# Performance work log

Hardware: AMD Instinct MI355X
Metric: run time of the kernel (lower is better)

Reference implementation:

```python
import jax, jax.numpy as jnp
import numpy as np

NUM_HEAD = 16
MODEL_DIM = 1024
K_DIM = MODEL_DIM // NUM_HEAD
LN_EPS = 1e-5


def setup_inputs() -> dict:
    key = jax.random.key(0)
    ks = jax.random.split(key, 9)
    B, N, D = 4, 2048, MODEL_DIM
    scale = 1.0 / np.sqrt(D)
    return {
        "q": jax.random.normal(ks[0], (B, N, D), dtype=jnp.float32),
        "k": jax.random.normal(ks[1], (B, N, D), dtype=jnp.float32),
        "v": jax.random.normal(ks[2], (B, N, D), dtype=jnp.float32),
        "Wq": jax.random.normal(ks[3], (D, D), dtype=jnp.float32) * scale,
        "Wk": jax.random.normal(ks[4], (D, D), dtype=jnp.float32) * scale,
        "Wv": jax.random.normal(ks[5], (D, D), dtype=jnp.float32) * scale,
        "Wo": jax.random.normal(ks[6], (D, D), dtype=jnp.float32) * scale,
        "gamma": jnp.ones((D,), dtype=jnp.float32),
        "beta": jnp.zeros((D,), dtype=jnp.float32),
    }


def reference(q, k, v, Wq, Wk, Wv, Wo, gamma, beta):
    B, N, D = q.shape
    H, Dh = NUM_HEAD, K_DIM
    # QKV projections (torch Linear: x @ W.T), then split heads -> [B,H,N,Dh]
    qs = (q @ Wq.T).reshape(B, N, H, Dh).transpose(0, 2, 1, 3)
    ks = (k @ Wk.T).reshape(B, N, H, Dh).transpose(0, 2, 1, 3)
    vs = (v @ Wv.T).reshape(B, N, H, Dh).transpose(0, 2, 1, 3)
    # scaled dot-product attention
    scores = jnp.einsum("bhqd,bhkd->bhqk", qs, ks) / jnp.sqrt(jnp.float32(Dh))
    probs = jax.nn.softmax(scores, axis=-1)
    attn = jnp.einsum("bhqk,bhkd->bhqd", probs, vs)
    # merge heads and output projection
    attn = attn.transpose(0, 2, 1, 3).reshape(B, N, D)
    out = attn @ Wo.T + q  # residual
    # LayerNorm
    mu = jnp.mean(out, axis=-1, keepdims=True)
    var = jnp.var(out, axis=-1, keepdims=True)
    out = (out - mu) * jax.lax.rsqrt(var + LN_EPS) * gamma + beta
    return out
```

## Files before the change

kernel.cpp:

```cpp
#include <hip/hip_runtime.h>
#include <cstdint>
#include <math.h>

typedef __bf16 bf16x8 __attribute__((ext_vector_type(8)));
typedef float f32x2 __attribute__((ext_vector_type(2)));
typedef float f32x4 __attribute__((ext_vector_type(4)));
typedef float f32x16 __attribute__((ext_vector_type(16)));
typedef int i32x2 __attribute__((ext_vector_type(2)));
typedef unsigned u32x4 __attribute__((ext_vector_type(4)));
typedef unsigned short u16;

#define B_ 4
#define N_ 2048
#define D_ 1024
#define H_ 16
#define DH_ 64
#define M_ (B_*N_)

#define QSCALE (0.125f * 1.44269504088896f)

typedef const void __attribute__((address_space(1))) gvoid;
typedef void __attribute__((address_space(3))) lvoid;

__device__ __forceinline__ void gload16(const void* g, void* l) {
  __builtin_amdgcn_global_load_lds((gvoid*)g, (lvoid*)l, 16, 0, 0);
}

__device__ __forceinline__ u16 cvt_bf(float f) {
  __bf16 h = (__bf16)f;
  return *(u16*)&h;
}

__device__ __forceinline__ unsigned cvt_pk(float lo, float hi) {
  unsigned r;
  asm("v_cvt_pk_bf16_f32 %0, %1, %2" : "=v"(r) : "v"(lo), "v"(hi));
  return r;
}

__device__ __forceinline__ i32x2 pl32swap(unsigned a, unsigned b) {
  return __builtin_amdgcn_permlane32_swap((int)a, (int)b, false, false);
}

__device__ __forceinline__ f32x2 pk_add(f32x2 a, f32x2 b) {
  f32x2 d;
  asm("v_pk_add_f32 %0, %1, %2" : "=v"(d) : "v"(a), "v"(b));
  return d;
}
__device__ __forceinline__ f32x2 pk_mul(f32x2 a, f32x2 b) {
  f32x2 d;
  asm("v_pk_mul_f32 %0, %1, %2" : "=v"(d) : "v"(a), "v"(b));
  return d;
}

__global__ __launch_bounds__(256) void cast_all(
    const float* __restrict__ q, const float* __restrict__ k, const float* __restrict__ v,
    const float* __restrict__ wq, const float* __restrict__ wk,
    const float* __restrict__ wv, const float* __restrict__ wo,
    u16* __restrict__ oq, u16* __restrict__ ok, u16* __restrict__ ov,
    u16* __restrict__ owq, u16* __restrict__ owk, u16* __restrict__ owv, u16* __restrict__ owo) {
  const int nb = (B_*N_*D_)/4;
  const int nw = (D_*D_)/4;
  int i = blockIdx.x * 256 + threadIdx.x;
  const float* s; u16* d;
  if (i < 3*nb) {
    if (i < nb)        { s = q; d = oq; }
    else if (i < 2*nb) { s = k; d = ok; i -= nb; }
    else               { s = v; d = ov; i -= 2*nb; }
  } else {
    i -= 3*nb;
    if (i < nw)        { s = wq; d = owq; }
    else if (i < 2*nw) { s = wk; d = owk; i -= nw; }
    else if (i < 3*nw) { s = wv; d = owv; i -= 2*nw; }
    else               { s = wo; d = owo; i -= 3*nw; }
  }
  float4 x = ((const float4*)s)[i];
  ushort4 y;
  y.x = cvt_bf(x.x); y.y = cvt_bf(x.y); y.z = cvt_bf(x.z); y.w = cvt_bf(x.w);
  ((ushort4*)d)[i] = y;
}

__global__ __launch_bounds__(256) void gemm_qkv(
    const u16* __restrict__ Aq, const u16* __restrict__ Ak, const u16* __restrict__ Av,
    const u16* __restrict__ Wq, const u16* __restrict__ Wk, const u16* __restrict__ Wv,
    u16* __restrict__ Oq, u16* __restrict__ Ok, u16* __restrict__ Ov)
{
  __shared__ __align__(16) u16 As[128*64];
  __shared__ __align__(16) u16 Bs[128*64];
  const int z = blockIdx.z;
  const u16* A = (z == 0) ? Aq : (z == 1) ? Ak : Av;
  const u16* W = (z == 0) ? Wq : (z == 1) ? Wk : Wv;
  u16* obf     = (z == 0) ? Oq : (z == 1) ? Ok : Ov;
  const float oscale = (z == 0) ? QSCALE : 1.0f;

  const int t = threadIdx.x;
  const int lane = t & 63;
  const int w = t >> 6;
  const int wr = w >> 1, wc = w & 1;
  const int m0 = blockIdx.x * 128;
  const int n0 = blockIdx.y * 128;
  f32x4 acc[4][4] = {};

  const int srow = t >> 3;
  const int scb = (t & 7) ^ (srow & 7);
  const int fr = lane & 15;
  const int fg = lane >> 4;
  const int fs7 = fr & 7;

  for (int k0 = 0; k0 < 1024; k0 += 64) {
#pragma unroll
    for (int p = 0; p < 4; ++p) {
      int r = p*32 + srow;
      gload16(A + (size_t)(m0 + r)*1024 + k0 + scb*8, &As[(p*256 + t)*8]);
      gload16(W + (size_t)(n0 + r)*1024 + k0 + scb*8, &Bs[(p*256 + t)*8]);
    }
    __syncthreads();
#pragma unroll
    for (int ks = 0; ks < 2; ++ks) {
      bf16x8 af[4], bfr[4];
#pragma unroll
      for (int i = 0; i < 4; ++i) {
        int ra = wr*64 + i*16 + fr;
        af[i]  = *(const bf16x8*)&As[ra*64 + (((ks*4 + fg) ^ fs7) * 8)];
        int rb = wc*64 + i*16 + fr;
        bfr[i] = *(const bf16x8*)&Bs[rb*64 + (((ks*4 + fg) ^ fs7) * 8)];
      }
#pragma unroll
      for (int i = 0; i < 4; ++i)
#pragma unroll
        for (int j = 0; j < 4; ++j)
          acc[i][j] = __builtin_amdgcn_mfma_f32_16x16x32_bf16(af[i], bfr[j], acc[i][j], 0, 0, 0);
    }
    __syncthreads();
  }

#pragma unroll
  for (int i = 0; i < 4; ++i) {
#pragma unroll
    for (int j = 0; j < 4; ++j) {
#pragma unroll
      for (int jj = 0; jj < 4; ++jj) {
        int row = m0 + wr*64 + i*16 + fg*4 + jj;
        int col = n0 + wc*64 + j*16 + fr;
        float val = acc[i][j][jj];
        int b = row >> 11, n = row & 2047, h = col >> 6, dh = col & 63;
        if (z != 2) {
          obf[(((size_t)(b*H_ + h))*N_ + n)*DH_ + dh] = cvt_bf(val * oscale);
        } else {
          obf[(((size_t)(b*H_ + h))*DH_ + dh)*N_ + n] = cvt_bf(val);
        }
      }
    }
  }
}

__global__ __launch_bounds__(256) void gemm_out(
    const u16* __restrict__ A, const u16* __restrict__ W,
    const float* __restrict__ resid, float* __restrict__ ofp)
{
  __shared__ __align__(16) u16 As[128*64];
  __shared__ __align__(16) u16 Bs[128*64];
  const int t = threadIdx.x;
  const int lane = t & 63;
  const int w = t >> 6;
  const int wr = w >> 1, wc = w & 1;
  const int m0 = blockIdx.x * 128;
  const int n0 = blockIdx.y * 128;
  f32x4 acc[4][4] = {};

  const int srow = t >> 3;
  const int scb = (t & 7) ^ (srow & 7);
  const int fr = lane & 15;
  const int fg = lane >> 4;
  const int fs7 = fr & 7;

  for (int k0 = 0; k0 < 1024; k0 += 64) {
#pragma unroll
    for (int p = 0; p < 4; ++p) {
      int r = p*32 + srow;
      gload16(A + (size_t)(m0 + r)*1024 + k0 + scb*8, &As[(p*256 + t)*8]);
      gload16(W + (size_t)(n0 + r)*1024 + k0 + scb*8, &Bs[(p*256 + t)*8]);
    }
    __syncthreads();
#pragma unroll
    for (int ks = 0; ks < 2; ++ks) {
      bf16x8 af[4], bfr[4];
#pragma unroll
      for (int i = 0; i < 4; ++i) {
        int ra = wr*64 + i*16 + fr;
        af[i]  = *(const bf16x8*)&As[ra*64 + (((ks*4 + fg) ^ fs7) * 8)];
        int rb = wc*64 + i*16 + fr;
        bfr[i] = *(const bf16x8*)&Bs[rb*64 + (((ks*4 + fg) ^ fs7) * 8)];
      }
#pragma unroll
      for (int i = 0; i < 4; ++i)
#pragma unroll
        for (int j = 0; j < 4; ++j)
          acc[i][j] = __builtin_amdgcn_mfma_f32_16x16x32_bf16(af[i], bfr[j], acc[i][j], 0, 0, 0);
    }
    __syncthreads();
  }

#pragma unroll
  for (int i = 0; i < 4; ++i)
#pragma unroll
    for (int j = 0; j < 4; ++j)
#pragma unroll
      for (int jj = 0; jj < 4; ++jj) {
        int row = m0 + wr*64 + i*16 + fg*4 + jj;
        int col = n0 + wc*64 + j*16 + fr;
        size_t idx = (size_t)row*1024 + col;
        ofp[idx] = acc[i][j][jj] + resid[idx];
      }
}

__device__ __forceinline__ f32x2 sp2(const f32x16& S, int i) {
  f32x2 r; r.x = S[2*i]; r.y = S[2*i + 1]; return r;
}
__device__ __forceinline__ void exp2v(f32x16& S) {
#pragma unroll
  for (int r = 0; r < 16; ++r) S[r] = __builtin_amdgcn_exp2f(S[r]);
}
__device__ __forceinline__ f32x2 sumtree(const f32x16& S0, const f32x16& S1) {
  f32x2 a0 = pk_add(sp2(S0,0), sp2(S0,1));
  f32x2 a1 = pk_add(sp2(S0,2), sp2(S0,3));
  f32x2 a2 = pk_add(sp2(S0,4), sp2(S0,5));
  f32x2 a3 = pk_add(sp2(S0,6), sp2(S0,7));
  f32x2 b0 = pk_add(sp2(S1,0), sp2(S1,1));
  f32x2 b1 = pk_add(sp2(S1,2), sp2(S1,3));
  f32x2 b2 = pk_add(sp2(S1,4), sp2(S1,5));
  f32x2 b3 = pk_add(sp2(S1,6), sp2(S1,7));
  a0 = pk_add(a0, a1); a2 = pk_add(a2, a3);
  b0 = pk_add(b0, b1); b2 = pk_add(b2, b3);
  a0 = pk_add(a0, a2); b0 = pk_add(b0, b2);
  return pk_add(a0, b0);
}
__device__ __forceinline__ void buildP(const f32x16& S, bf16x8* pf) {
  unsigned w0 = cvt_pk(S[0], S[1]),  w1 = cvt_pk(S[2], S[3]);
  unsigned w2 = cvt_pk(S[4], S[5]),  w3 = cvt_pk(S[6], S[7]);
  i32x2 A2 = pl32swap(w0, w2), B2 = pl32swap(w1, w3);
  u32x4 f0 = { (unsigned)A2.x, (unsigned)B2.x, (unsigned)A2.y, (unsigned)B2.y };
  pf[0] = __builtin_bit_cast(bf16x8, f0);
  unsigned w4 = cvt_pk(S[8], S[9]),   w5 = cvt_pk(S[10], S[11]);
  unsigned w6 = cvt_pk(S[12], S[13]), w7 = cvt_pk(S[14], S[15]);
  i32x2 C2 = pl32swap(w4, w6), D2 = pl32swap(w5, w7);
  u32x4 f1 = { (unsigned)C2.x, (unsigned)D2.x, (unsigned)C2.y, (unsigned)D2.y };
  pf[1] = __builtin_bit_cast(bf16x8, f1);
}

__global__ __launch_bounds__(256, 2) void flash_attn(
    const u16* __restrict__ Qs, const u16* __restrict__ Ks,
    const u16* __restrict__ VTs, u16* __restrict__ ctx)
{
  __shared__ __align__(16) u16 Klds[2][64*64];
  __shared__ __align__(16) u16 Vlds[2][64*64];
  const int t = threadIdx.x;
  const int lane = t & 63;
  const int w = t >> 6;
  const int l31 = lane & 31;
  const int h = lane >> 5;
  const int bh = blockIdx.x;
  const int q0 = blockIdx.y * 256 + w * 64;
  const u16* Qbh = Qs  + (size_t)bh * N_ * DH_;
  const u16* Kbh = Ks  + (size_t)bh * N_ * DH_;
  const u16* Vbh = VTs + (size_t)bh * DH_ * N_;

  bf16x8 qfA[4], qfB[4];
#pragma unroll
  for (int dd = 0; dd < 4; ++dd) {
    qfA[dd] = *(const bf16x8*)&Qbh[(size_t)(q0 + l31)*64 + dd*16 + h*8];
    qfB[dd] = *(const bf16x8*)&Qbh[(size_t)(q0 + 32 + l31)*64 + dd*16 + h*8];
  }

  f32x2 lA = {0.f, 0.f}, lB = {0.f, 0.f};
  f32x16 OA0 = {}, OA1 = {}, OB0 = {}, OB1 = {};

  const int srow = t >> 3;
  const int scb  = (t & 7) ^ (srow & 7);
  const u16* ksrc = Kbh + (size_t)srow*64 + scb*8;
  const u16* vsrc = Vbh + (size_t)srow*N_ + scb*8;

  auto stage = [&](int buf, int kv) {
#pragma unroll
    for (int p = 0; p < 2; ++p) {
      gload16(ksrc + (size_t)(kv + p*32)*64, &Klds[buf][(p*256 + t)*8]);
      gload16(vsrc + kv + (size_t)(p*32)*N_, &Vlds[buf][(p*256 + t)*8]);
    }
  };

  const int l7 = l31 & 7;

  stage(0, 0);
  __syncthreads();
  int cur = 0;

  for (int kv0 = 0; kv0 < N_; kv0 += 64) {
    if (kv0 + 64 < N_) stage(cur ^ 1, kv0 + 64);

    bf16x8 kf0[4], kf1[4];
#pragma unroll
    for (int dd = 0; dd < 4; ++dd) {
      int cb = ((dd*2 + h) ^ l7) * 8;
      kf0[dd] = *(const bf16x8*)&Klds[cur][l31*64 + cb];
      kf1[dd] = *(const bf16x8*)&Klds[cur][(32 + l31)*64 + cb];
    }
    f32x16 SA0 = {}, SA1 = {}, SB0 = {}, SB1 = {};
    __builtin_amdgcn_s_setprio(1);
#pragma unroll
    for (int dd = 0; dd < 4; ++dd) {
      SA0 = __builtin_amdgcn_mfma_f32_32x32x16_bf16(kf0[dd], qfA[dd], SA0, 0, 0, 0);
      SA1 = __builtin_amdgcn_mfma_f32_32x32x16_bf16(kf1[dd], qfA[dd], SA1, 0, 0, 0);
    }
#pragma unroll
    for (int dd = 0; dd < 4; ++dd) {
      SB0 = __builtin_amdgcn_mfma_f32_32x32x16_bf16(kf0[dd], qfB[dd], SB0, 0, 0, 0);
      SB1 = __builtin_amdgcn_mfma_f32_32x32x16_bf16(kf1[dd], qfB[dd], SB1, 0, 0, 0);
    }
    __builtin_amdgcn_s_setprio(0);

    exp2v(SA0); exp2v(SA1);
    bf16x8 pfA[4];
    buildP(SA0, &pfA[0]);
    buildP(SA1, &pfA[2]);

    bf16x8 vf0[4], vf1[4];
#pragma unroll
    for (int ks = 0; ks < 4; ++ks) {
      int cb = ((ks*2 + h) ^ l7) * 8;
      vf0[ks] = *(const bf16x8*)&Vlds[cur][l31*64 + cb];
      vf1[ks] = *(const bf16x8*)&Vlds[cur][(32 + l31)*64 + cb];
    }
    __builtin_amdgcn_s_setprio(1);
#pragma unroll
    for (int ks = 0; ks < 4; ++ks) {
      OA0 = __builtin_amdgcn_mfma_f32_32x32x16_bf16(vf0[ks], pfA[ks], OA0, 0, 0, 0);
      OA1 = __builtin_amdgcn_mfma_f32_32x32x16_bf16(vf1[ks], pfA[ks], OA1, 0, 0, 0);
    }
    __builtin_amdgcn_s_setprio(0);
    lA = pk_add(lA, sumtree(SA0, SA1));

    exp2v(SB0); exp2v(SB1);
    bf16x8 pfB[4];
    buildP(SB0, &pfB[0]);
    buildP(SB1, &pfB[2]);
    __builtin_amdgcn_s_setprio(1);
#pragma unroll
    for (int ks = 0; ks < 4; ++ks) {
      OB0 = __builtin_amdgcn_mfma_f32_32x32x16_bf16(vf0[ks], pfB[ks], OB0, 0, 0, 0);
      OB1 = __builtin_amdgcn_mfma_f32_32x32x16_bf16(vf1[ks], pfB[ks], OB1, 0, 0, 0);
    }
    __builtin_amdgcn_s_setprio(0);
    lB = pk_add(lB, sumtree(SB0, SB1));

    __syncthreads();
    cur ^= 1;
  }

  int b = bh >> 4, hh = bh & 15;
  {
    float lps = lA.x + lA.y;
    i32x2 lsw = pl32swap(__float_as_uint(lps), __float_as_uint(lps));
    float ltot = __uint_as_float((unsigned)lsw.x) + __uint_as_float((unsigned)lsw.y);
    float linv = __builtin_amdgcn_rcpf(ltot);
    f32x2 li2; li2.x = linv; li2.y = linv;
    unsigned* crow = (unsigned*)(ctx + ((size_t)b*N_ + (q0 + l31))*D_ + hh*64);
#pragma unroll
    for (int rp = 0; rp < 8; ++rp) {
      int r = rp*2;
      int d0 = (r & 3) + 8*(r >> 2) + 4*h;
      f32x2 o0 = pk_mul(sp2(OA0, rp), li2);
      f32x2 o1 = pk_mul(sp2(OA1, rp), li2);
      crow[d0 >> 1]        = cvt_pk(o0.x, o0.y);
      crow[(d0 + 32) >> 1] = cvt_pk(o1.x, o1.y);
    }
  }
  {
    float lps = lB.x + lB.y;
    i32x2 lsw = pl32swap(__float_as_uint(lps), __float_as_uint(lps));
    float ltot = __uint_as_float((unsigned)lsw.x) + __uint_as_float((unsigned)lsw.y);
    float linv = __builtin_amdgcn_rcpf(ltot);
    f32x2 li2; li2.x = linv; li2.y = linv;
    unsigned* crow = (unsigned*)(ctx + ((size_t)b*N_ + (q0 + 32 + l31))*D_ + hh*64);
#pragma unroll
    for (int rp = 0; rp < 8; ++rp) {
      int r = rp*2;
      int d0 = (r & 3) + 8*(r >> 2) + 4*h;
      f32x2 o0 = pk_mul(sp2(OB0, rp), li2);
      f32x2 o1 = pk_mul(sp2(OB1, rp), li2);
      crow[d0 >> 1]        = cvt_pk(o0.x, o0.y);
      crow[(d0 + 32) >> 1] = cvt_pk(o1.x, o1.y);
    }
  }
}

__global__ __launch_bounds__(256) void ln_fwd(float* __restrict__ io,
    const float* __restrict__ gamma, const float* __restrict__ beta)
{
  __shared__ float red[4];
  const int t = threadIdx.x;
  const int lane = t & 63, w = t >> 6;
  float4* row = (float4*)(io + (size_t)blockIdx.x * 1024);
  float4 x = row[t];
  float s = x.x + x.y + x.z + x.w;
#pragma unroll
  for (int m = 1; m < 64; m <<= 1) s += __shfl_xor(s, m);
  if (lane == 0) red[w] = s;
  __syncthreads();
  float mean = (red[0] + red[1] + red[2] + red[3]) * (1.f/1024.f);
  __syncthreads();
  float dx0 = x.x - mean, dx1 = x.y - mean, dx2 = x.z - mean, dx3 = x.w - mean;
  float sq = dx0*dx0 + dx1*dx1 + dx2*dx2 + dx3*dx3;
#pragma unroll
  for (int m = 1; m < 64; m <<= 1) sq += __shfl_xor(sq, m);
  if (lane == 0) red[w] = sq;
  __syncthreads();
  float var = (red[0] + red[1] + red[2] + red[3]) * (1.f/1024.f);
  float rstd = rsqrtf(var + 1e-5f);
  float4 g = ((const float4*)gamma)[t];
  float4 bb = ((const float4*)beta)[t];
  float4 y;
  y.x = dx0*rstd*g.x + bb.x;
  y.y = dx1*rstd*g.y + bb.y;
  y.z = dx2*rstd*g.z + bb.z;
  y.w = dx3*rstd*g.w + bb.w;
  row[t] = y;
}

extern "C" void kernel_launch(void* const* d_in, const int* in_sizes, int n_in,
                              void* d_out, int out_size, void* d_ws, size_t ws_size,
                              hipStream_t stream) {
  const float* q     = (const float*)d_in[0];
  const float* k     = (const float*)d_in[1];
  const float* v     = (const float*)d_in[2];
  const float* Wq    = (const float*)d_in[3];
  const float* Wk    = (const float*)d_in[4];
  const float* Wv    = (const float*)d_in[5];
  const float* Wo    = (const float*)d_in[6];
  const float* gamma = (const float*)d_in[7];
  const float* beta  = (const float*)d_in[8];
  float* out = (float*)d_out;

  char* ws = (char*)d_ws;
  const size_t MB = 1024*1024;
  u16* qb  = (u16*)(ws + 0*MB);
  u16* kb  = (u16*)(ws + 16*MB);
  u16* vb  = (u16*)(ws + 32*MB);
  u16* Wqb = (u16*)(ws + 48*MB);
  u16* Wkb = (u16*)(ws + 50*MB);
  u16* Wvb = (u16*)(ws + 52*MB);
  u16* Wob = (u16*)(ws + 54*MB);
  u16* Qs  = (u16*)(ws + 56*MB);
  u16* Ks  = (u16*)(ws + 72*MB);
  u16* VTs = (u16*)(ws + 88*MB);
  u16* ctx = (u16*)(ws + 0*MB);

  const int ntot4 = 3*((B_*N_*D_)/4) + 4*((D_*D_)/4);
  cast_all<<<ntot4/256, 256, 0, stream>>>(q, k, v, Wq, Wk, Wv, Wo,
                                          qb, kb, vb, Wqb, Wkb, Wvb, Wob);

  dim3 gproj(M_/128, D_/128, 3);
  gemm_qkv<<<gproj, 256, 0, stream>>>(qb, kb, vb, Wqb, Wkb, Wvb, Qs, Ks, VTs);

  flash_attn<<<dim3(B_*H_, N_/256), 256, 0, stream>>>(Qs, Ks, VTs, ctx);

  gemm_out<<<dim3(M_/128, D_/128), 256, 0, stream>>>(ctx, Wob, q, out);

  ln_fwd<<<M_, 256, 0, stream>>>(out, gamma, beta);
}
```

Before: 223.6 us.

## Fuse fp32 activation cast into QKV GEMM and double flash-attn KV tile

Removes the separate bf16 cast of q/k/v activations: the QKV GEMM now loads fp32 A tiles into LDS and converts to bf16 when building MFMA fragments, so only the weights are cast up front. This skips writing and re-reading about 48MB of bf16 copies, at the cost of twice the A-tile LDS traffic and extra convert instructions inside the GEMM inner loop. Separately, flash attention now stages 128 keys per iteration instead of 64, halving barrier count at the cost of double the LDS footprint, which may reduce occupancy.

```diff
diff --git a/kernel.cpp b/kernel.cpp
--- a/kernel.cpp
+++ b/kernel.cpp
@@ -52,27 +52,17 @@
   return d;
 }
 
-__global__ __launch_bounds__(256) void cast_all(
-    const float* __restrict__ q, const float* __restrict__ k, const float* __restrict__ v,
-    const float* __restrict__ wq, const float* __restrict__ wk,
-    const float* __restrict__ wv, const float* __restrict__ wo,
-    u16* __restrict__ oq, u16* __restrict__ ok, u16* __restrict__ ov,
-    u16* __restrict__ owq, u16* __restrict__ owk, u16* __restrict__ owv, u16* __restrict__ owo) {
-  const int nb = (B_*N_*D_)/4;
+__global__ __launch_bounds__(256) void cast_w(
+    const float* __restrict__ a, const float* __restrict__ b,
+    const float* __restrict__ c, const float* __restrict__ e,
+    u16* __restrict__ oa, u16* __restrict__ ob, u16* __restrict__ oc, u16* __restrict__ oe) {
   const int nw = (D_*D_)/4;
   int i = blockIdx.x * 256 + threadIdx.x;
   const float* s; u16* d;
-  if (i < 3*nb) {
-    if (i < nb)        { s = q; d = oq; }
-    else if (i < 2*nb) { s = k; d = ok; i -= nb; }
-    else               { s = v; d = ov; i -= 2*nb; }
-  } else {
-    i -= 3*nb;
-    if (i < nw)        { s = wq; d = owq; }
-    else if (i < 2*nw) { s = wk; d = owk; i -= nw; }
-    else if (i < 3*nw) { s = wv; d = owv; i -= 2*nw; }
-    else               { s = wo; d = owo; i -= 3*nw; }
-  }
+  if (i < nw)        { s = a; d = oa; }
+  else if (i < 2*nw) { s = b; d = ob; i -= nw; }
+  else if (i < 3*nw) { s = c; d = oc; i -= 2*nw; }
+  else               { s = e; d = oe; i -= 3*nw; }
   float4 x = ((const float4*)s)[i];
   ushort4 y;
   y.x = cvt_bf(x.x); y.y = cvt_bf(x.y); y.z = cvt_bf(x.z); y.w = cvt_bf(x.w);
@@ -80,16 +70,16 @@
 }
 
 __global__ __launch_bounds__(256) void gemm_qkv(
-    const u16* __restrict__ Aq, const u16* __restrict__ Ak, const u16* __restrict__ Av,
+    const float* __restrict__ Aq, const float* __restrict__ Ak, const float* __restrict__ Av,
     const u16* __restrict__ Wq, const u16* __restrict__ Wk, const u16* __restrict__ Wv,
     u16* __restrict__ Oq, u16* __restrict__ Ok, u16* __restrict__ Ov)
 {
-  __shared__ __align__(16) u16 As[128*64];
+  __shared__ __align__(16) float As32[128*64];
   __shared__ __align__(16) u16 Bs[128*64];
   const int z = blockIdx.z;
-  const u16* A = (z == 0) ? Aq : (z == 1) ? Ak : Av;
-  const u16* W = (z == 0) ? Wq : (z == 1) ? Wk : Wv;
-  u16* obf     = (z == 0) ? Oq : (z == 1) ? Ok : Ov;
+  const float* A = (z == 0) ? Aq : (z == 1) ? Ak : Av;
+  const u16* W  = (z == 0) ? Wq : (z == 1) ? Wk : Wv;
+  u16* obf      = (z == 0) ? Oq : (z == 1) ? Ok : Ov;
   const float oscale = (z == 0) ? QSCALE : 1.0f;
 
   const int t = threadIdx.x;
@@ -102,17 +92,20 @@
 
   const int srow = t >> 3;
   const int scb = (t & 7) ^ (srow & 7);
+  const int arow = t >> 4;
+  const int asb  = (t & 15) ^ arow;
+
   const int fr = lane & 15;
   const int fg = lane >> 4;
   const int fs7 = fr & 7;
 
   for (int k0 = 0; k0 < 1024; k0 += 64) {
 #pragma unroll
-    for (int p = 0; p < 4; ++p) {
-      int r = p*32 + srow;
-      gload16(A + (size_t)(m0 + r)*1024 + k0 + scb*8, &As[(p*256 + t)*8]);
-      gload16(W + (size_t)(n0 + r)*1024 + k0 + scb*8, &Bs[(p*256 + t)*8]);
-    }
+    for (int p = 0; p < 4; ++p)
+      gload16(W + (size_t)(n0 + p*32 + srow)*1024 + k0 + scb*8, &Bs[(p*256 + t)*8]);
+#pragma unroll
+    for (int p = 0; p < 8; ++p)
+      gload16(A + (size_t)(m0 + p*16 + arow)*1024 + k0 + asb*4, &As32[(p*256 + t)*4]);
     __syncthreads();
 #pragma unroll
     for (int ks = 0; ks < 2; ++ks) {
@@ -120,7 +113,13 @@
 #pragma unroll
       for (int i = 0; i < 4; ++i) {
         int ra = wr*64 + i*16 + fr;
-        af[i]  = *(const bf16x8*)&As[ra*64 + (((ks*4 + fg) ^ fs7) * 8)];
+        int b0 = (ks*4 + fg) * 2;
+        int r15 = ra & 15;
+        f32x4 lo = *(const f32x4*)&As32[ra*64 + ((b0 ^ r15) * 4)];
+        f32x4 hi = *(const f32x4*)&As32[ra*64 + (((b0 + 1) ^ r15) * 4)];
+        u32x4 pk = { cvt_pk(lo.x, lo.y), cvt_pk(lo.z, lo.w),
+                     cvt_pk(hi.x, hi.y), cvt_pk(hi.z, hi.w) };
+        af[i] = __builtin_bit_cast(bf16x8, pk);
         int rb = wc*64 + i*16 + fr;
         bfr[i] = *(const bf16x8*)&Bs[rb*64 + (((ks*4 + fg) ^ fs7) * 8)];
       }
@@ -251,8 +250,8 @@
     const u16* __restrict__ Qs, const u16* __restrict__ Ks,
     const u16* __restrict__ VTs, u16* __restrict__ ctx)
 {
-  __shared__ __align__(16) u16 Klds[2][64*64];
-  __shared__ __align__(16) u16 Vlds[2][64*64];
+  __shared__ __align__(16) u16 Klds[2][128*64];
+  __shared__ __align__(16) u16 Vlds[2][64*128];
   const int t = threadIdx.x;
   const int lane = t & 63;
   const int w = t >> 6;
@@ -274,82 +273,90 @@
   f32x2 lA = {0.f, 0.f}, lB = {0.f, 0.f};
   f32x16 OA0 = {}, OA1 = {}, OB0 = {}, OB1 = {};
 
-  const int srow = t >> 3;
-  const int scb  = (t & 7) ^ (srow & 7);
-  const u16* ksrc = Kbh + (size_t)srow*64 + scb*8;
-  const u16* vsrc = Vbh + (size_t)srow*N_ + scb*8;
+  const int krow = t >> 3;
+  const int kcb  = (t & 7) ^ (krow & 7);
+  const int vrow = t >> 4;
+  const int vcb  = (t & 15) ^ vrow;
+  const u16* ksrc = Kbh + (size_t)krow*64 + kcb*8;
+  const u16* vsrc = Vbh + (size_t)vrow*N_ + vcb*8;
 
   auto stage = [&](int buf, int kv) {
 #pragma unroll
-    for (int p = 0; p < 2; ++p) {
+    for (int p = 0; p < 4; ++p)
       gload16(ksrc + (size_t)(kv + p*32)*64, &Klds[buf][(p*256 + t)*8]);
-      gload16(vsrc + kv + (size_t)(p*32)*N_, &Vlds[buf][(p*256 + t)*8]);
-    }
+#pragma unroll
+    for (int p = 0; p < 4; ++p)
+      gload16(vsrc + kv + (size_t)(p*16)*N_, &Vlds[buf][(p*256 + t)*8]);
   };
 
   const int l7 = l31 & 7;
+  const int l15 = l31 & 15;
 
   stage(0, 0);
   __syncthreads();
   int cur = 0;
 
-  for (int kv0 = 0; kv0 < N_; kv0 += 64) {
-    if (kv0 + 64 < N_) stage(cur ^ 1, kv0 + 64);
-
-    bf16x8 kf0[4], kf1[4];
-#pragma unroll
-    for (int dd = 0; dd < 4; ++dd) {
-      int cb = ((dd*2 + h) ^ l7) * 8;
-      kf0[dd] = *(const bf16x8*)&Klds[cur][l31*64 + cb];
-      kf1[dd] = *(const bf16x8*)&Klds[cur][(32 + l31)*64 + cb];
-    }
-    f32x16 SA0 = {}, SA1 = {}, SB0 = {}, SB1 = {};
-    __builtin_amdgcn_s_setprio(1);
-#pragma unroll
-    for (int dd = 0; dd < 4; ++dd) {
-      SA0 = __builtin_amdgcn_mfma_f32_32x32x16_bf16(kf0[dd], qfA[dd], SA0, 0, 0, 0);
-      SA1 = __builtin_amdgcn_mfma_f32_32x32x16_bf16(kf1[dd], qfA[dd], SA1, 0, 0, 0);
-    }
-#pragma unroll
-    for (int dd = 0; dd < 4; ++dd) {
-      SB0 = __builtin_amdgcn_mfma_f32_32x32x16_bf16(kf0[dd], qfB[dd], SB0, 0, 0, 0);
-      SB1 = __builtin_amdgcn_mfma_f32_32x32x16_bf16(kf1[dd], qfB[dd], SB1, 0, 0, 0);
-    }
-    __builtin_amdgcn_s_setprio(0);
-
-    exp2v(SA0); exp2v(SA1);
-    bf16x8 pfA[4];
-    buildP(SA0, &pfA[0]);
-    buildP(SA1, &pfA[2]);
-
-    bf16x8 vf0[4], vf1[4];
-#pragma unroll
-    for (int ks = 0; ks < 4; ++ks) {
-      int cb = ((ks*2 + h) ^ l7) * 8;
-      vf0[ks] = *(const bf16x8*)&Vlds[cur][l31*64 + cb];
-      vf1[ks] = *(const bf16x8*)&Vlds[cur][(32 + l31)*64 + cb];
-    }
-    __builtin_amdgcn_s_setprio(1);
-#pragma unroll
-    for (int ks = 0; ks < 4; ++ks) {
-      OA0 = __builtin_amdgcn_mfma_f32_32x32x16_bf16(vf0[ks], pfA[ks], OA0, 0, 0, 0);
-      OA1 = __builtin_amdgcn_mfma_f32_32x32x16_bf16(vf1[ks], pfA[ks], OA1, 0, 0, 0);
-    }
-    __builtin_amdgcn_s_setprio(0);
-    lA = pk_add(lA, sumtree(SA0, SA1));
-
-    exp2v(SB0); exp2v(SB1);
-    bf16x8 pfB[4];
-    buildP(SB0, &pfB[0]);
-    buildP(SB1, &pfB[2]);
-    __builtin_amdgcn_s_setprio(1);
-#pragma unroll
-    for (int ks = 0; ks < 4; ++ks) {
-      OB0 = __builtin_amdgcn_mfma_f32_32x32x16_bf16(vf0[ks], pfB[ks], OB0, 0, 0, 0);
-      OB1 = __builtin_amdgcn_mfma_f32_32x32x16_bf16(vf1[ks], pfB[ks], OB1, 0, 0, 0);
-    }
-    __builtin_amdgcn_s_setprio(0);
-    lB = pk_add(lB, sumtree(SB0, SB1));
+  for (int kv0 = 0; kv0 < N_; kv0 += 128) {
+    if (kv0 + 128 < N_) stage(cur ^ 1, kv0 + 128);
+
+#pragma unroll
+    for (int c = 0; c < 2; ++c) {
+      const int kb = c * 64;
+      bf16x8 kf0[4], kf1[4];
+#pragma unroll
+      for (int dd = 0; dd < 4; ++dd) {
+        int cb = ((dd*2 + h) ^ l7) * 8;
+        kf0[dd] = *(const bf16x8*)&Klds[cur][(kb + l31)*64 + cb];
+        kf1[dd] = *(const bf16x8*)&Klds[cur][(kb + 32 + l31)*64 + cb];
+      }
+      f32x16 SA0 = {}, SA1 = {}, SB0 = {}, SB1 = {};
+      __builtin_amdgcn_s_setprio(1);
+#pragma unroll
+      for (int dd = 0; dd < 4; ++dd) {
+        SA0 = __builtin_amdgcn_mfma_f32_32x32x16_bf16(kf0[dd], qfA[dd], SA0, 0, 0, 0);
+        SA1 = __builtin_amdgcn_mfma_f32_32x32x16_bf16(kf1[dd], qfA[dd], SA1, 0, 0, 0);
+      }
+#pragma unroll
+      for (int dd = 0; dd < 4; ++dd) {
+        SB0 = __builtin_amdgcn_mfma_f32_32x32x16_bf16(kf0[dd], qfB[dd], SB0, 0, 0, 0);
+        SB1 = __builtin_amdgcn_mfma_f32_32x32x16_bf16(kf1[dd], qfB[dd], SB1, 0, 0, 0);
+      }
+      __builtin_amdgcn_s_setprio(0);
+
+      exp2v(SA0); exp2v(SA1);
+      bf16x8 pfA[4];
+      buildP(SA0, &pfA[0]);
+      buildP(SA1, &pfA[2]);
+
+      bf16x8 vf0[4], vf1[4];
+#pragma unroll
+      for (int ks = 0; ks < 4; ++ks) {
+        int kc = (c*8 + ks*2 + h) ^ l15;
+        vf0[ks] = *(const bf16x8*)&Vlds[cur][l31*128 + kc*8];
+        vf1[ks] = *(const bf16x8*)&Vlds[cur][(32 + l31)*128 + kc*8];
+      }
+      __builtin_amdgcn_s_setprio(1);
+#pragma unroll
+      for (int ks = 0; ks < 4; ++ks) {
+        OA0 = __builtin_amdgcn_mfma_f32_32x32x16_bf16(vf0[ks], pfA[ks], OA0, 0, 0, 0);
+        OA1 = __builtin_amdgcn_mfma_f32_32x32x16_bf16(vf1[ks], pfA[ks], OA1, 0, 0, 0);
+      }
+      __builtin_amdgcn_s_setprio(0);
+      lA = pk_add(lA, sumtree(SA0, SA1));
+
+      exp2v(SB0); exp2v(SB1);
+      bf16x8 pfB[4];
+      buildP(SB0, &pfB[0]);
+      buildP(SB1, &pfB[2]);
+      __builtin_amdgcn_s_setprio(1);
+#pragma unroll
+      for (int ks = 0; ks < 4; ++ks) {
+        OB0 = __builtin_amdgcn_mfma_f32_32x32x16_bf16(vf0[ks], pfB[ks], OB0, 0, 0, 0);
+        OB1 = __builtin_amdgcn_mfma_f32_32x32x16_bf16(vf1[ks], pfB[ks], OB1, 0, 0, 0);
+      }
+      __builtin_amdgcn_s_setprio(0);
+      lB = pk_add(lB, sumtree(SB0, SB1));
+    }
 
     __syncthreads();
     cur ^= 1;
@@ -441,24 +448,20 @@
 
   char* ws = (char*)d_ws;
   const size_t MB = 1024*1024;
-  u16* qb  = (u16*)(ws + 0*MB);
-  u16* kb  = (u16*)(ws + 16*MB);
-  u16* vb  = (u16*)(ws + 32*MB);
-  u16* Wqb = (u16*)(ws + 48*MB);
-  u16* Wkb = (u16*)(ws + 50*MB);
-  u16* Wvb = (u16*)(ws + 52*MB);
-  u16* Wob = (u16*)(ws + 54*MB);
-  u16* Qs  = (u16*)(ws + 56*MB);
-  u16* Ks  = (u16*)(ws + 72*MB);
-  u16* VTs = (u16*)(ws + 88*MB);
-  u16* ctx = (u16*)(ws + 0*MB);
-
-  const int ntot4 = 3*((B_*N_*D_)/4) + 4*((D_*D_)/4);
-  cast_all<<<ntot4/256, 256, 0, stream>>>(q, k, v, Wq, Wk, Wv, Wo,
-                                          qb, kb, vb, Wqb, Wkb, Wvb, Wob);
+  u16* Wqb = (u16*)(ws + 0*MB);
+  u16* Wkb = (u16*)(ws + 2*MB);
+  u16* Wvb = (u16*)(ws + 4*MB);
+  u16* Wob = (u16*)(ws + 6*MB);
+  u16* Qs  = (u16*)(ws + 8*MB);
+  u16* Ks  = (u16*)(ws + 24*MB);
+  u16* VTs = (u16*)(ws + 40*MB);
+  u16* ctx = (u16*)(ws + 56*MB);
+
+  const int nw4 = 4*((D_*D_)/4);
+  cast_w<<<nw4/256, 256, 0, stream>>>(Wq, Wk, Wv, Wo, Wqb, Wkb, Wvb, Wob);
 
   dim3 gproj(M_/128, D_/128, 3);
-  gemm_qkv<<<gproj, 256, 0, stream>>>(qb, kb, vb, Wqb, Wkb, Wvb, Qs, Ks, VTs);
+  gemm_qkv<<<gproj, 256, 0, stream>>>(q, k, v, Wqb, Wkb, Wvb, Qs, Ks, VTs);
 
   flash_attn<<<dim3(B_*H_, N_/256), 256, 0, stream>>>(Qs, Ks, VTs, ctx);
 
```

After: 212.4 us. 1.05x faster.

## Double-buffer GEMM LDS tiles and widen flash-attention KV tile to 128

Applied to the files above, without the earlier changes.

The QKV and output projection GEMMs now double-buffer their LDS tiles, so the loads for the next K slice are issued while the current slice is multiplied, and they get a launch bound of two blocks per CU. The flash-attention kernel stages 128 keys per iteration instead of 64, with the V tile relaid to 128-wide rows and a 16-way XOR swizzle. It processes each tile in two 64-key sub-chunks, which halves the number of barriers. The cost is double the LDS footprint in every kernel (64KB per GEMM block, 64KB per attention block), which may limit occupancy.

```diff
diff --git a/kernel.cpp b/kernel.cpp
--- a/kernel.cpp
+++ b/kernel.cpp
@@ -79,13 +79,13 @@
   ((ushort4*)d)[i] = y;
 }
 
-__global__ __launch_bounds__(256) void gemm_qkv(
+__global__ __launch_bounds__(256, 2) void gemm_qkv(
     const u16* __restrict__ Aq, const u16* __restrict__ Ak, const u16* __restrict__ Av,
     const u16* __restrict__ Wq, const u16* __restrict__ Wk, const u16* __restrict__ Wv,
     u16* __restrict__ Oq, u16* __restrict__ Ok, u16* __restrict__ Ov)
 {
-  __shared__ __align__(16) u16 As[128*64];
-  __shared__ __align__(16) u16 Bs[128*64];
+  __shared__ __align__(16) u16 As[2][128*64];
+  __shared__ __align__(16) u16 Bs[2][128*64];
   const int z = blockIdx.z;
   const u16* A = (z == 0) ? Aq : (z == 1) ? Ak : Av;
   const u16* W = (z == 0) ? Wq : (z == 1) ? Wk : Wv;
@@ -106,23 +106,32 @@
   const int fg = lane >> 4;
   const int fs7 = fr & 7;
 
+  const u16* asrc = A + (size_t)(m0 + srow)*1024 + scb*8;
+  const u16* wsrc = W + (size_t)(n0 + srow)*1024 + scb*8;
+
+  auto stage = [&](int buf, int k0) {
+#pragma unroll
+    for (int p = 0; p < 4; ++p) {
+      gload16(asrc + (size_t)(p*32)*1024 + k0, &As[buf][(p*256 + t)*8]);
+      gload16(wsrc + (size_t)(p*32)*1024 + k0, &Bs[buf][(p*256 + t)*8]);
+    }
+  };
+
+  stage(0, 0);
+  __syncthreads();
+  int cur = 0;
+
   for (int k0 = 0; k0 < 1024; k0 += 64) {
-#pragma unroll
-    for (int p = 0; p < 4; ++p) {
-      int r = p*32 + srow;
-      gload16(A + (size_t)(m0 + r)*1024 + k0 + scb*8, &As[(p*256 + t)*8]);
-      gload16(W + (size_t)(n0 + r)*1024 + k0 + scb*8, &Bs[(p*256 + t)*8]);
-    }
-    __syncthreads();
+    if (k0 + 64 < 1024) stage(cur ^ 1, k0 + 64);
 #pragma unroll
     for (int ks = 0; ks < 2; ++ks) {
       bf16x8 af[4], bfr[4];
 #pragma unroll
       for (int i = 0; i < 4; ++i) {
         int ra = wr*64 + i*16 + fr;
-        af[i]  = *(const bf16x8*)&As[ra*64 + (((ks*4 + fg) ^ fs7) * 8)];
+        af[i]  = *(const bf16x8*)&As[cur][ra*64 + (((ks*4 + fg) ^ fs7) * 8)];
         int rb = wc*64 + i*16 + fr;
-        bfr[i] = *(const bf16x8*)&Bs[rb*64 + (((ks*4 + fg) ^ fs7) * 8)];
+        bfr[i] = *(const bf16x8*)&Bs[cur][rb*64 + (((ks*4 + fg) ^ fs7) * 8)];
       }
 #pragma unroll
       for (int i = 0; i < 4; ++i)
@@ -131,6 +140,7 @@
           acc[i][j] = __builtin_amdgcn_mfma_f32_16x16x32_bf16(af[i], bfr[j], acc[i][j], 0, 0, 0);
     }
     __syncthreads();
+    cur ^= 1;
   }
 
 #pragma unroll
@@ -153,12 +163,12 @@
   }
 }
 
-__global__ __launch_bounds__(256) void gemm_out(
+__global__ __launch_bounds__(256, 2) void gemm_out(
     const u16* __restrict__ A, const u16* __restrict__ W,
     const float* __restrict__ resid, float* __restrict__ ofp)
 {
-  __shared__ __align__(16) u16 As[128*64];
-  __shared__ __align__(16) u16 Bs[128*64];
+  __shared__ __align__(16) u16 As[2][128*64];
+  __shared__ __align__(16) u16 Bs[2][128*64];
   const int t = threadIdx.x;
   const int lane = t & 63;
   const int w = t >> 6;
@@ -173,23 +183,32 @@
   const int fg = lane >> 4;
   const int fs7 = fr & 7;
 
+  const u16* asrc = A + (size_t)(m0 + srow)*1024 + scb*8;
+  const u16* wsrc = W + (size_t)(n0 + srow)*1024 + scb*8;
+
+  auto stage = [&](int buf, int k0) {
+#pragma unroll
+    for (int p = 0; p < 4; ++p) {
+      gload16(asrc + (size_t)(p*32)*1024 + k0, &As[buf][(p*256 + t)*8]);
+      gload16(wsrc + (size_t)(p*32)*1024 + k0, &Bs[buf][(p*256 + t)*8]);
+    }
+  };
+
+  stage(0, 0);
+  __syncthreads();
+  int cur = 0;
+
   for (int k0 = 0; k0 < 1024; k0 += 64) {
-#pragma unroll
-    for (int p = 0; p < 4; ++p) {
-      int r = p*32 + srow;
-      gload16(A + (size_t)(m0 + r)*1024 + k0 + scb*8, &As[(p*256 + t)*8]);
-      gload16(W + (size_t)(n0 + r)*1024 + k0 + scb*8, &Bs[(p*256 + t)*8]);
-    }
-    __syncthreads();
+    if (k0 + 64 < 1024) stage(cur ^ 1, k0 + 64);
 #pragma unroll
     for (int ks = 0; ks < 2; ++ks) {
       bf16x8 af[4], bfr[4];
 #pragma unroll
       for (int i = 0; i < 4; ++i) {
         int ra = wr*64 + i*16 + fr;
-        af[i]  = *(const bf16x8*)&As[ra*64 + (((ks*4 + fg) ^ fs7) * 8)];
+        af[i]  = *(const bf16x8*)&As[cur][ra*64 + (((ks*4 + fg) ^ fs7) * 8)];
         int rb = wc*64 + i*16 + fr;
-        bfr[i] = *(const bf16x8*)&Bs[rb*64 + (((ks*4 + fg) ^ fs7) * 8)];
+        bfr[i] = *(const bf16x8*)&Bs[cur][rb*64 + (((ks*4 + fg) ^ fs7) * 8)];
       }
 #pragma unroll
       for (int i = 0; i < 4; ++i)
@@ -198,6 +217,7 @@
           acc[i][j] = __builtin_amdgcn_mfma_f32_16x16x32_bf16(af[i], bfr[j], acc[i][j], 0, 0, 0);
     }
     __syncthreads();
+    cur ^= 1;
   }
 
 #pragma unroll
@@ -251,8 +271,8 @@
     const u16* __restrict__ Qs, const u16* __restrict__ Ks,
     const u16* __restrict__ VTs, u16* __restrict__ ctx)
 {
-  __shared__ __align__(16) u16 Klds[2][64*64];
-  __shared__ __align__(16) u16 Vlds[2][64*64];
+  __shared__ __align__(16) u16 Klds[2][128*64];
+  __shared__ __align__(16) u16 Vlds[2][64*128];
   const int t = threadIdx.x;
   const int lane = t & 63;
   const int w = t >> 6;
@@ -274,82 +294,90 @@
   f32x2 lA = {0.f, 0.f}, lB = {0.f, 0.f};
   f32x16 OA0 = {}, OA1 = {}, OB0 = {}, OB1 = {};
 
-  const int srow = t >> 3;
-  const int scb  = (t & 7) ^ (srow & 7);
-  const u16* ksrc = Kbh + (size_t)srow*64 + scb*8;
-  const u16* vsrc = Vbh + (size_t)srow*N_ + scb*8;
+  const int krow = t >> 3;
+  const int kcb  = (t & 7) ^ (krow & 7);
+  const int vrow = t >> 4;
+  const int vcb  = (t & 15) ^ vrow;
+  const u16* ksrc = Kbh + (size_t)krow*64 + kcb*8;
+  const u16* vsrc = Vbh + (size_t)vrow*N_ + vcb*8;
 
   auto stage = [&](int buf, int kv) {
 #pragma unroll
-    for (int p = 0; p < 2; ++p) {
+    for (int p = 0; p < 4; ++p)
       gload16(ksrc + (size_t)(kv + p*32)*64, &Klds[buf][(p*256 + t)*8]);
-      gload16(vsrc + kv + (size_t)(p*32)*N_, &Vlds[buf][(p*256 + t)*8]);
-    }
+#pragma unroll
+    for (int p = 0; p < 4; ++p)
+      gload16(vsrc + kv + (size_t)(p*16)*N_, &Vlds[buf][(p*256 + t)*8]);
   };
 
   const int l7 = l31 & 7;
+  const int l15 = l31 & 15;
 
   stage(0, 0);
   __syncthreads();
   int cur = 0;
 
-  for (int kv0 = 0; kv0 < N_; kv0 += 64) {
-    if (kv0 + 64 < N_) stage(cur ^ 1, kv0 + 64);
-
-    bf16x8 kf0[4], kf1[4];
-#pragma unroll
-    for (int dd = 0; dd < 4; ++dd) {
-      int cb = ((dd*2 + h) ^ l7) * 8;
-      kf0[dd] = *(const bf16x8*)&Klds[cur][l31*64 + cb];
-      kf1[dd] = *(const bf16x8*)&Klds[cur][(32 + l31)*64 + cb];
-    }
-    f32x16 SA0 = {}, SA1 = {}, SB0 = {}, SB1 = {};
-    __builtin_amdgcn_s_setprio(1);
-#pragma unroll
-    for (int dd = 0; dd < 4; ++dd) {
-      SA0 = __builtin_amdgcn_mfma_f32_32x32x16_bf16(kf0[dd], qfA[dd], SA0, 0, 0, 0);
-      SA1 = __builtin_amdgcn_mfma_f32_32x32x16_bf16(kf1[dd], qfA[dd], SA1, 0, 0, 0);
-    }
-#pragma unroll
-    for (int dd = 0; dd < 4; ++dd) {
-      SB0 = __builtin_amdgcn_mfma_f32_32x32x16_bf16(kf0[dd], qfB[dd], SB0, 0, 0, 0);
-      SB1 = __builtin_amdgcn_mfma_f32_32x32x16_bf16(kf1[dd], qfB[dd], SB1, 0, 0, 0);
-    }
-    __builtin_amdgcn_s_setprio(0);
-
-    exp2v(SA0); exp2v(SA1);
-    bf16x8 pfA[4];
-    buildP(SA0, &pfA[0]);
-    buildP(SA1, &pfA[2]);
-
-    bf16x8 vf0[4], vf1[4];
-#pragma unroll
-    for (int ks = 0; ks < 4; ++ks) {
-      int cb = ((ks*2 + h) ^ l7) * 8;
-      vf0[ks] = *(const bf16x8*)&Vlds[cur][l31*64 + cb];
-      vf1[ks] = *(const bf16x8*)&Vlds[cur][(32 + l31)*64 + cb];
-    }
-    __builtin_amdgcn_s_setprio(1);
-#pragma unroll
-    for (int ks = 0; ks < 4; ++ks) {
-      OA0 = __builtin_amdgcn_mfma_f32_32x32x16_bf16(vf0[ks], pfA[ks], OA0, 0, 0, 0);
-      OA1 = __builtin_amdgcn_mfma_f32_32x32x16_bf16(vf1[ks], pfA[ks], OA1, 0, 0, 0);
-    }
-    __builtin_amdgcn_s_setprio(0);
-    lA = pk_add(lA, sumtree(SA0, SA1));
-
-    exp2v(SB0); exp2v(SB1);
-    bf16x8 pfB[4];
-    buildP(SB0, &pfB[0]);
-    buildP(SB1, &pfB[2]);
-    __builtin_amdgcn_s_setprio(1);
-#pragma unroll
-    for (int ks = 0; ks < 4; ++ks) {
-      OB0 = __builtin_amdgcn_mfma_f32_32x32x16_bf16(vf0[ks], pfB[ks], OB0, 0, 0, 0);
-      OB1 = __builtin_amdgcn_mfma_f32_32x32x16_bf16(vf1[ks], pfB[ks], OB1, 0, 0, 0);
-    }
-    __builtin_amdgcn_s_setprio(0);
-    lB = pk_add(lB, sumtree(SB0, SB1));
+  for (int kv0 = 0; kv0 < N_; kv0 += 128) {
+    if (kv0 + 128 < N_) stage(cur ^ 1, kv0 + 128);
+
+#pragma unroll
+    for (int c = 0; c < 2; ++c) {
+      const int kb = c * 64;
+      bf16x8 kf0[4], kf1[4];
+#pragma unroll
+      for (int dd = 0; dd < 4; ++dd) {
+        int cb = ((dd*2 + h) ^ l7) * 8;
+        kf0[dd] = *(const bf16x8*)&Klds[cur][(kb + l31)*64 + cb];
+        kf1[dd] = *(const bf16x8*)&Klds[cur][(kb + 32 + l31)*64 + cb];
+      }
+      f32x16 SA0 = {}, SA1 = {}, SB0 = {}, SB1 = {};
+      __builtin_amdgcn_s_setprio(1);
+#pragma unroll
+      for (int dd = 0; dd < 4; ++dd) {
+        SA0 = __builtin_amdgcn_mfma_f32_32x32x16_bf16(kf0[dd], qfA[dd], SA0, 0, 0, 0);
+        SA1 = __builtin_amdgcn_mfma_f32_32x32x16_bf16(kf1[dd], qfA[dd], SA1, 0, 0, 0);
+      }
+#pragma unroll
+      for (int dd = 0; dd < 4; ++dd) {
+        SB0 = __builtin_amdgcn_mfma_f32_32x32x16_bf16(kf0[dd], qfB[dd], SB0, 0, 0, 0);
+        SB1 = __builtin_amdgcn_mfma_f32_32x32x16_bf16(kf1[dd], qfB[dd], SB1, 0, 0, 0);
+      }
+      __builtin_amdgcn_s_setprio(0);
+
+      exp2v(SA0); exp2v(SA1);
+      bf16x8 pfA[4];
+      buildP(SA0, &pfA[0]);
+      buildP(SA1, &pfA[2]);
+
+      bf16x8 vf0[4], vf1[4];
+#pragma unroll
+      for (int ks = 0; ks < 4; ++ks) {
+        int kc = (c*8 + ks*2 + h) ^ l15;
+        vf0[ks] = *(const bf16x8*)&Vlds[cur][l31*128 + kc*8];
+        vf1[ks] = *(const bf16x8*)&Vlds[cur][(32 + l31)*128 + kc*8];
+      }
+      __builtin_amdgcn_s_setprio(1);
+#pragma unroll
+      for (int ks = 0; ks < 4; ++ks) {
+        OA0 = __builtin_amdgcn_mfma_f32_32x32x16_bf16(vf0[ks], pfA[ks], OA0, 0, 0, 0);
+        OA1 = __builtin_amdgcn_mfma_f32_32x32x16_bf16(vf1[ks], pfA[ks], OA1, 0, 0, 0);
+      }
+      __builtin_amdgcn_s_setprio(0);
+      lA = pk_add(lA, sumtree(SA0, SA1));
+
+      exp2v(SB0); exp2v(SB1);
+      bf16x8 pfB[4];
+      buildP(SB0, &pfB[0]);
+      buildP(SB1, &pfB[2]);
+      __builtin_amdgcn_s_setprio(1);
+#pragma unroll
+      for (int ks = 0; ks < 4; ++ks) {
+        OB0 = __builtin_amdgcn_mfma_f32_32x32x16_bf16(vf0[ks], pfB[ks], OB0, 0, 0, 0);
+        OB1 = __builtin_amdgcn_mfma_f32_32x32x16_bf16(vf1[ks], pfB[ks], OB1, 0, 0, 0);
+      }
+      __builtin_amdgcn_s_setprio(0);
+      lB = pk_add(lB, sumtree(SB0, SB1));
+    }
 
     __syncthreads();
     cur ^= 1;
```

New measurement: 223.4 us. No clear change (-0.1%).
